# Optimization experiments

Measured on AMD Instinct MI355X. Metric: run time of the kernel, lower is better.

The kernel has to match this reference:

```python
import jax, jax.numpy as jnp
import numpy as np

MID = 256

def setup_inputs() -> dict:
    key = jax.random.key(0)
    ks = jax.random.split(key, 6)
    s = 1.0 / np.sqrt(MID)
    u = lambda k, shape: jax.random.uniform(k, shape, jnp.float32, -s, s)
    return {
        "W_ih": u(ks[0], (4 * MID, 2)),
        "W_hh": u(ks[1], (4 * MID, MID)),
        "b_ih": u(ks[2], (4 * MID,)),
        "b_hh": u(ks[3], (4 * MID,)),
        "W_out": u(ks[4], (1, MID)),
        "b_out": u(ks[5], (1,)),
        "sequence_dim": 48,
        "sequence_num": 512,
    }

def reference(W_ih, W_hh, b_ih, b_hh, W_out, b_out, sequence_dim, sequence_num):
    # obs is 2-D -> torch nn.LSTM treats it as UNBATCHED: (L=sequence_num, H_in=2),
    # hidden state (mid,) per layer, carried across outer iterations.
    N = sequence_num
    mid = W_hh.shape[1]
    b = b_ih + b_hh  # fuse the two LSTM biases

    def lstm(hc, obs):
        # obs: (N, 2) time-major unbatched sequence
        def step(carry, x):
            h, c = carry
            g = W_ih @ x + W_hh @ h + b          # (4*mid,)
            i, f, gg, o = jnp.split(g, 4)         # torch gate order i,f,g,o
            c = jax.nn.sigmoid(f) * c + jax.nn.sigmoid(i) * jnp.tanh(gg)
            h = jax.nn.sigmoid(o) * jnp.tanh(c)
            return (h, c), h
        hc, hs = jax.lax.scan(step, hc, obs)
        return hc, hs                              # hs: (N, mid)

    def outer(carry, k):
        hc, samp, prob = carry
        obs = jnp.concatenate([samp, prob], axis=1)  # (N, 2)
        hc, hs = lstm(hc, obs)
        p = jax.nn.sigmoid(hs @ W_out.T + b_out)     # (N, 1)
        smp = jax.random.bernoulli(k, p).astype(p.dtype)
        lp = smp * jnp.log(p) + (1.0 - smp) * jnp.log1p(-p)        # Bernoulli log_prob
        ent = -(p * jnp.log(p) + (1.0 - p) * jnp.log1p(-p))        # Bernoulli entropy
        return (hc, smp, p), (smp[:, 0], lp[:, 0], ent[:, 0])

    key = jax.random.key(42)
    keys = jax.random.split(key, sequence_dim - 1)
    h0 = (jnp.zeros((mid,), W_hh.dtype), jnp.zeros((mid,), W_hh.dtype))
    z = jnp.zeros((N, 1), W_hh.dtype)
    _, (ss, lps, ents) = jax.lax.scan(outer, (h0, z, z), keys)

    samples = jnp.concatenate([jnp.zeros((1, N), ss.dtype), ss], axis=0)  # (T, N)
    samples = samples.T.astype(jnp.int32)                                  # (N, T)
    logprobs = lps.sum(0)
    logprobs = logprobs - logprobs.mean()
    entropies = ents.mean(0)
    return samples, logprobs, entropies
```

## Files before the change

### kernel.cpp

```cpp
#include <hip/hip_runtime.h>
#include <stdint.h>


#define MID      256
#define NOUT     48
#define NSEQ     512
#define NOUTER   47
#define NSTEP    (NOUTER * NSEQ)
#define NBLK     16
#define MAGIC_V  0x1234ABCDu
#define LOG2E    1.4426950408889634f

__device__ __forceinline__ uint32_t rotl32(uint32_t x, int d) {
  return (x << d) | (x >> (32 - d));
}

__device__ __forceinline__ void threefry2x32(uint32_t k0, uint32_t k1,
                                             uint32_t x0, uint32_t x1,
                                             uint32_t& o0, uint32_t& o1) {
  uint32_t ks2 = k0 ^ k1 ^ 0x1BD11BDAu;
  uint32_t v0 = x0 + k0, v1 = x1 + k1;
#define TF_R(r) { v0 += v1; v1 = rotl32(v1, r); v1 ^= v0; }
  TF_R(13) TF_R(15) TF_R(26) TF_R(6)
  v0 += k1;  v1 += ks2 + 1u;
  TF_R(17) TF_R(29) TF_R(16) TF_R(24)
  v0 += ks2; v1 += k0 + 2u;
  TF_R(13) TF_R(15) TF_R(26) TF_R(6)
  v0 += k0;  v1 += k1 + 3u;
  TF_R(17) TF_R(29) TF_R(16) TF_R(24)
  v0 += k1;  v1 += ks2 + 4u;
  TF_R(13) TF_R(15) TF_R(26) TF_R(6)
  v0 += ks2; v1 += k0 + 5u;
#undef TF_R
  o0 = v0; o1 = v1;
}

__device__ __forceinline__ float sigf(float x) { return 1.0f / (1.0f + expf(-x)); }

__device__ __forceinline__ uint64_t packht(float h, uint32_t tag) {
  return ((uint64_t)tag << 32) | (uint64_t)__float_as_uint(h);
}

__global__ __launch_bounds__(256, 1)
void arlstm_kernel(const float* __restrict__ W_ih, const float* __restrict__ W_hh,
                   const float* __restrict__ b_ih, const float* __restrict__ b_hh,
                   const float* __restrict__ W_out, const float* __restrict__ b_out,
                   float* __restrict__ out, uint64_t* __restrict__ ws) {
  uint64_t* h_hist = ws;
  float*    obsbuf = (float*)(ws + 512 * 256);
  uint32_t* p_prog = (uint32_t*)(obsbuf + 2 * 512 * 2);
  uint32_t* magic  = p_prog + 16;

  const int tid = threadIdx.x;
  const int blk = blockIdx.x;

  __shared__ __align__(16) float hstage[256];
  __shared__ float plds[4][64];
  __shared__ float obs_lds[2];
  __shared__ float lp_acc[512];
  __shared__ float ent_acc[512];
  __shared__ float red[256];

  if (blk == NBLK) {
    __hip_atomic_store(&h_hist[tid], 0ull, __ATOMIC_RELAXED, __HIP_MEMORY_SCOPE_AGENT);
    if (tid < 16)
      __hip_atomic_store(&p_prog[tid], 0u, __ATOMIC_RELAXED, __HIP_MEMORY_SCOPE_AGENT);
    out[(tid)       * NOUT] = 0.0f;
    out[(tid + 256) * NOUT] = 0.0f;
    lp_acc[tid] = 0.0f;  lp_acc[tid + 256] = 0.0f;
    ent_acc[tid] = 0.0f; ent_acc[tid + 256] = 0.0f;
    __threadfence();
    __syncthreads();
    if (tid == 0)
      __hip_atomic_store(magic, MAGIC_V, __ATOMIC_RELEASE, __HIP_MEMORY_SCOPE_AGENT);

    const int w    = tid >> 6;
    const int lane = tid & 63;
    const float wo0 = W_out[lane * 4 + 0], wo1 = W_out[lane * 4 + 1];
    const float wo2 = W_out[lane * 4 + 2], wo3 = W_out[lane * 4 + 3];
    const float bo = b_out[0];

    for (int s = w + 1; s <= NSTEP; s += 4) {
      const int k = (s - 1) >> 9;
      const int t = (s - 1) & 511;
      uint64_t* src = h_hist + (uint64_t)(s & 511) * 256 + lane * 4;
      uint64_t v0, v1, v2, v3;
      for (;;) {
        v0 = __hip_atomic_load(src + 0, __ATOMIC_RELAXED, __HIP_MEMORY_SCOPE_AGENT);
        v1 = __hip_atomic_load(src + 1, __ATOMIC_RELAXED, __HIP_MEMORY_SCOPE_AGENT);
        v2 = __hip_atomic_load(src + 2, __ATOMIC_RELAXED, __HIP_MEMORY_SCOPE_AGENT);
        v3 = __hip_atomic_load(src + 3, __ATOMIC_RELAXED, __HIP_MEMORY_SCOPE_AGENT);
        int ok = ((uint32_t)(v0 >> 32) == (uint32_t)s) &
                 ((uint32_t)(v1 >> 32) == (uint32_t)s) &
                 ((uint32_t)(v2 >> 32) == (uint32_t)s) &
                 ((uint32_t)(v3 >> 32) == (uint32_t)s);
        if (__all(ok)) break;
      }
      float zp = fmaf(__uint_as_float((uint32_t)v0), wo0,
                 fmaf(__uint_as_float((uint32_t)v1), wo1,
                 fmaf(__uint_as_float((uint32_t)v2), wo2,
                      __uint_as_float((uint32_t)v3) * wo3)));
      zp += __shfl_xor(zp, 1);
      zp += __shfl_xor(zp, 2);
      zp += __shfl_xor(zp, 4);
      zp += __shfl_xor(zp, 8);
      zp += __shfl_xor(zp, 16);
      zp += __shfl_xor(zp, 32);
      const float p = sigf(zp + bo);

      uint32_t ka, kb, c1, c2;
      threefry2x32(0u, 42u, 0u, (uint32_t)k, ka, kb);
      threefry2x32(ka, kb, 0u, (uint32_t)t, c1, c2);
      const uint32_t bits = c1 ^ c2;
      const float u = __uint_as_float((bits >> 9) | 0x3f800000u) - 1.0f;
      const float smp = (u < p) ? 1.0f : 0.0f;

      if (lane == 0) {
        uint32_t* ob = (uint32_t*)(obsbuf + ((k + 1) & 1) * (512 * 2) + t * 2);
        __hip_atomic_store(&ob[0], __float_as_uint(smp), __ATOMIC_RELAXED, __HIP_MEMORY_SCOPE_AGENT);
        __hip_atomic_store(&ob[1], __float_as_uint(p),   __ATOMIC_RELAXED, __HIP_MEMORY_SCOPE_AGENT);
        __hip_atomic_store(&p_prog[w], (uint32_t)s, __ATOMIC_RELEASE, __HIP_MEMORY_SCOPE_AGENT);
        out[t * NOUT + (k + 1)] = smp;
        const float lg = logf(p), lg1 = log1pf(-p);
        lp_acc[t]  += (smp > 0.5f) ? lg : lg1;
        ent_acc[t] -= (p * lg + (1.0f - p) * lg1);
      }
    }
    __syncthreads();
    red[tid] = lp_acc[tid] + lp_acc[tid + 256];
    __syncthreads();
    for (int off = 128; off > 0; off >>= 1) {
      if (tid < off) red[tid] += red[tid + off];
      __syncthreads();
    }
    const float mean = red[0] * (1.0f / 512.0f);
    out[24576 + tid]        = lp_acc[tid]        - mean;
    out[24576 + 256 + tid]  = lp_acc[tid + 256]  - mean;
    out[25088 + tid]        = ent_acc[tid]       * (1.0f / 47.0f);
    out[25088 + 256 + tid]  = ent_acc[tid + 256] * (1.0f / 47.0f);
  } else {
    const int part = tid >> 6;
    const int r    = tid & 63;
    const int gate = r >> 4;
    const int jloc = r & 15;
    const int row  = gate * 256 + blk * 16 + jloc;

    float wreg[64];
#pragma unroll
    for (int c = 0; c < 64; ++c)
      wreg[c] = W_hh[row * 256 + part * 64 + c];

    float bb = 0.f, wx0 = 0.f, wx1 = 0.f, mconst = 0.f, ml = 0.f, ad = 0.f;
    if (tid < 64) {
      const int g4 = tid >> 4;
      const int rr = g4 * 256 + blk * 16 + (tid & 15);
      bb  = b_ih[rr] + b_hh[rr];
      wx0 = W_ih[rr * 2 + 0];
      wx1 = W_ih[rr * 2 + 1];
      mconst = (g4 == 2) ? (-2.0f * LOG2E) : (-LOG2E);
      ml     = (g4 == 2) ? 2.0f : 1.0f;
      ad     = (g4 == 2) ? -1.0f : 0.0f;
    }

    if (tid == 0) {
      while (__hip_atomic_load(magic, __ATOMIC_ACQUIRE, __HIP_MEMORY_SCOPE_AGENT) != MAGIC_V) {}
    }
    __syncthreads();

    float c_st = 0.0f;
    const int jglob = blk * 16 + (tid & 15);

    for (int s = 1; s <= NSTEP; ++s) {
      const int k = (s - 1) >> 9;
      const int t = (s - 1) & 511;

      float samp = 0.0f, pv = 0.0f;
      if (tid == 255 && k > 0) {
        const uint32_t X = (uint32_t)((k - 1) * 512 + t + 1);
        while (__hip_atomic_load(&p_prog[t & 3], __ATOMIC_ACQUIRE, __HIP_MEMORY_SCOPE_AGENT) < X) {}
        uint32_t* ob = (uint32_t*)(obsbuf + (k & 1) * (512 * 2) + t * 2);
        samp = __uint_as_float(__hip_atomic_load(&ob[0], __ATOMIC_RELAXED, __HIP_MEMORY_SCOPE_AGENT));
        pv   = __uint_as_float(__hip_atomic_load(&ob[1], __ATOMIC_RELAXED, __HIP_MEMORY_SCOPE_AGENT));
      }

      {
        uint64_t* src = h_hist + (uint64_t)((s - 1) & 511) * 256 + tid;
        const uint32_t want = (uint32_t)(s - 1);
        uint64_t v = __hip_atomic_load(src, __ATOMIC_RELAXED, __HIP_MEMORY_SCOPE_AGENT);
        if ((uint32_t)(v >> 32) != want) {
          uint64_t a = __hip_atomic_load(src, __ATOMIC_RELAXED, __HIP_MEMORY_SCOPE_AGENT);
          uint64_t b = __hip_atomic_load(src, __ATOMIC_RELAXED, __HIP_MEMORY_SCOPE_AGENT);
          for (;;) {
            if ((uint32_t)(a >> 32) == want) { v = a; break; }
            a = __hip_atomic_load(src, __ATOMIC_RELAXED, __HIP_MEMORY_SCOPE_AGENT);
            if ((uint32_t)(b >> 32) == want) { v = b; break; }
            b = __hip_atomic_load(src, __ATOMIC_RELAXED, __HIP_MEMORY_SCOPE_AGENT);
          }
        }
        hstage[tid] = __uint_as_float((uint32_t)v);
      }
      if (tid == 255) { obs_lds[0] = samp; obs_lds[1] = pv; }
      __syncthreads();

      float a0 = 0.f, a1 = 0.f, a2 = 0.f, a3 = 0.f;
      const float4* hs4 = (const float4*)(hstage + part * 64);
#pragma unroll
      for (int i = 0; i < 16; ++i) {
        const float4 hv = hs4[i];
        a0 = fmaf(wreg[4 * i + 0], hv.x, a0);
        a1 = fmaf(wreg[4 * i + 1], hv.y, a1);
        a2 = fmaf(wreg[4 * i + 2], hv.z, a2);
        a3 = fmaf(wreg[4 * i + 3], hv.w, a3);
      }
      plds[part][r] = (a0 + a1) + (a2 + a3);
      __syncthreads();

      if (tid < 64) {
        const float sx = obs_lds[0], px = obs_lds[1];
        const float base = wx0 * sx + wx1 * px + bb;
        const float gv = ((plds[0][tid] + plds[1][tid]) +
                          (plds[2][tid] + plds[3][tid])) + base;
        const float e   = __builtin_amdgcn_exp2f(gv * mconst);
        const float y   = __builtin_amdgcn_rcpf(1.0f + e);
        const float act = __builtin_fmaf(ml, y, ad);
        const int j = tid & 15;
        const float a_f = __shfl(act, j + 16, 64);
        const float a_g = __shfl(act, j + 32, 64);
        const float a_o = __shfl(act, j + 48, 64);
        if (tid < 16) {
          const float t1 = a_f * c_st;
          const float t2 = act * a_g;
          c_st = t1 + t2;
          const float ec = __builtin_amdgcn_exp2f(c_st * (-2.0f * LOG2E));
          const float yc = __builtin_amdgcn_rcpf(1.0f + ec);
          const float th = __builtin_fmaf(2.0f, yc, -1.0f);
          const float hnew = a_o * th;
          __hip_atomic_store(&h_hist[(uint64_t)(s & 511) * 256 + jglob],
                             packht(hnew, (uint32_t)s),
                             __ATOMIC_RELAXED, __HIP_MEMORY_SCOPE_AGENT);
        }
      }
    }
  }
}

extern "C" void kernel_launch(void* const* d_in, const int* in_sizes, int n_in,
                              void* d_out, int out_size, void* d_ws, size_t ws_size,
                              hipStream_t stream) {
  const float* W_ih  = (const float*)d_in[0];
  const float* W_hh  = (const float*)d_in[1];
  const float* b_ih  = (const float*)d_in[2];
  const float* b_hh  = (const float*)d_in[3];
  const float* W_out = (const float*)d_in[4];
  const float* b_out = (const float*)d_in[5];
  float* out = (float*)d_out;
  uint64_t* ws = (uint64_t*)d_ws;

  arlstm_kernel<<<dim3(NBLK + 1), dim3(256), 0, stream>>>(
      W_ih, W_hh, b_ih, b_hh, W_out, b_out, out, ws);
}
```

Baseline: 31.76 ms.

## Spread LSTM recurrence over 64 single-wave blocks and add clock-warming spin blocks

The recurrent matvec is redistributed from 16 blocks of 256 threads to 64 blocks that each use one 64-lane wavefront for 4 hidden units. Each lane holds a quarter of a W_hh row in float4 registers and reduces across lanes with shuffles. This removes the per-step __syncthreads and the LDS partial-sum stage from the critical serial path, at the cost of 4x more blocks polling the shared h history. Separately, 96 extra blocks run busy FMA loops until the sampler signals completion, apparently to keep the GPU at a high clock state during the latency-bound recurrence. That adds power draw and depends on all blocks being co-resident.

```diff
diff --git a/kernel.cpp b/kernel.cpp
--- a/kernel.cpp
+++ b/kernel.cpp
@@ -7,9 +7,17 @@
 #define NSEQ     512
 #define NOUTER   47
 #define NSTEP    (NOUTER * NSEQ)
-#define NBLK     16
+#define NWRK     64
+#define SAMP_BLK 64
+#define NHEAT    96
 #define MAGIC_V  0x1234ABCDu
+#define DONE_V   0x0D0E0D0Eu
 #define LOG2E    1.4426950408889634f
+
+#define AL_RELAX(p)    __hip_atomic_load((p), __ATOMIC_RELAXED, __HIP_MEMORY_SCOPE_AGENT)
+#define AL_ACQ(p)      __hip_atomic_load((p), __ATOMIC_ACQUIRE, __HIP_MEMORY_SCOPE_AGENT)
+#define AS_RELAX(p, v) __hip_atomic_store((p), (v), __ATOMIC_RELAXED, __HIP_MEMORY_SCOPE_AGENT)
+#define AS_REL(p, v)   __hip_atomic_store((p), (v), __ATOMIC_RELEASE, __HIP_MEMORY_SCOPE_AGENT)
 
 __device__ __forceinline__ uint32_t rotl32(uint32_t x, int d) {
   return (x << d) | (x >> (32 - d));
@@ -50,29 +58,43 @@
   float*    obsbuf = (float*)(ws + 512 * 256);
   uint32_t* p_prog = (uint32_t*)(obsbuf + 2 * 512 * 2);
   uint32_t* magic  = p_prog + 16;
+  uint32_t* done   = p_prog + 17;
+  float*    heat   = (float*)(p_prog + 32);
 
   const int tid = threadIdx.x;
   const int blk = blockIdx.x;
 
-  __shared__ __align__(16) float hstage[256];
-  __shared__ float plds[4][64];
-  __shared__ float obs_lds[2];
+  __shared__ __align__(16) float4 hstage4[64];
   __shared__ float lp_acc[512];
   __shared__ float ent_acc[512];
   __shared__ float red[256];
 
-  if (blk == NBLK) {
-    __hip_atomic_store(&h_hist[tid], 0ull, __ATOMIC_RELAXED, __HIP_MEMORY_SCOPE_AGENT);
-    if (tid < 16)
-      __hip_atomic_store(&p_prog[tid], 0u, __ATOMIC_RELAXED, __HIP_MEMORY_SCOPE_AGENT);
+  if (blk >= NWRK + 1) {
+    float h0 = (float)tid * 1.1f + 0.1f, h1 = h0 + 0.7f, h2 = h0 + 1.3f, h3 = h0 + 2.9f;
+    const float ca = 1.0000001f, cb = 1e-7f;
+    while (AL_RELAX(done) != DONE_V) {
+#pragma unroll 64
+      for (int i = 0; i < 1024; ++i) {
+        h0 = __builtin_fmaf(h0, ca, cb);
+        h1 = __builtin_fmaf(h1, ca, cb);
+        h2 = __builtin_fmaf(h2, ca, cb);
+        h3 = __builtin_fmaf(h3, ca, cb);
+      }
+    }
+    if (tid == 0) heat[blk - NWRK - 1 + 0] = (h0 + h1) + (h2 + h3);
+    return;
+  }
+
+  if (blk == SAMP_BLK) {
+    AS_RELAX(&h_hist[tid], 0ull);
+    if (tid < 16) AS_RELAX(&p_prog[tid], 0u);
     out[(tid)       * NOUT] = 0.0f;
     out[(tid + 256) * NOUT] = 0.0f;
     lp_acc[tid] = 0.0f;  lp_acc[tid + 256] = 0.0f;
     ent_acc[tid] = 0.0f; ent_acc[tid + 256] = 0.0f;
     __threadfence();
     __syncthreads();
-    if (tid == 0)
-      __hip_atomic_store(magic, MAGIC_V, __ATOMIC_RELEASE, __HIP_MEMORY_SCOPE_AGENT);
+    if (tid == 0) AS_REL(magic, MAGIC_V);
 
     const int w    = tid >> 6;
     const int lane = tid & 63;
@@ -86,10 +108,10 @@
       uint64_t* src = h_hist + (uint64_t)(s & 511) * 256 + lane * 4;
       uint64_t v0, v1, v2, v3;
       for (;;) {
-        v0 = __hip_atomic_load(src + 0, __ATOMIC_RELAXED, __HIP_MEMORY_SCOPE_AGENT);
-        v1 = __hip_atomic_load(src + 1, __ATOMIC_RELAXED, __HIP_MEMORY_SCOPE_AGENT);
-        v2 = __hip_atomic_load(src + 2, __ATOMIC_RELAXED, __HIP_MEMORY_SCOPE_AGENT);
-        v3 = __hip_atomic_load(src + 3, __ATOMIC_RELAXED, __HIP_MEMORY_SCOPE_AGENT);
+        v0 = AL_RELAX(src + 0);
+        v1 = AL_RELAX(src + 1);
+        v2 = AL_RELAX(src + 2);
+        v3 = AL_RELAX(src + 3);
         int ok = ((uint32_t)(v0 >> 32) == (uint32_t)s) &
                  ((uint32_t)(v1 >> 32) == (uint32_t)s) &
                  ((uint32_t)(v2 >> 32) == (uint32_t)s) &
@@ -117,9 +139,9 @@
 
       if (lane == 0) {
         uint32_t* ob = (uint32_t*)(obsbuf + ((k + 1) & 1) * (512 * 2) + t * 2);
-        __hip_atomic_store(&ob[0], __float_as_uint(smp), __ATOMIC_RELAXED, __HIP_MEMORY_SCOPE_AGENT);
-        __hip_atomic_store(&ob[1], __float_as_uint(p),   __ATOMIC_RELAXED, __HIP_MEMORY_SCOPE_AGENT);
-        __hip_atomic_store(&p_prog[w], (uint32_t)s, __ATOMIC_RELEASE, __HIP_MEMORY_SCOPE_AGENT);
+        AS_RELAX(&ob[0], __float_as_uint(smp));
+        AS_RELAX(&ob[1], __float_as_uint(p));
+        AS_REL(&p_prog[w], (uint32_t)s);
         out[t * NOUT + (k + 1)] = smp;
         const float lg = logf(p), lg1 = log1pf(-p);
         lp_acc[t]  += (smp > 0.5f) ? lg : lg1;
@@ -138,108 +160,111 @@
     out[24576 + 256 + tid]  = lp_acc[tid + 256]  - mean;
     out[25088 + tid]        = ent_acc[tid]       * (1.0f / 47.0f);
     out[25088 + 256 + tid]  = ent_acc[tid + 256] * (1.0f / 47.0f);
-  } else {
-    const int part = tid >> 6;
-    const int r    = tid & 63;
-    const int gate = r >> 4;
-    const int jloc = r & 15;
-    const int row  = gate * 256 + blk * 16 + jloc;
-
-    float wreg[64];
+    __syncthreads();
+    if (tid == 0) { __threadfence(); AS_REL(done, DONE_V); }
+    return;
+  }
+
+  if (tid >= 64) return;
+  const int l  = tid;
+  const int g  = l >> 4;
+  const int jj = (l >> 2) & 3;
+  const int q  = l & 3;
+  const int u  = l >> 2;
+  const int row = g * 256 + blk * 4 + jj;
+
+  float4 wf[16];
 #pragma unroll
-    for (int c = 0; c < 64; ++c)
-      wreg[c] = W_hh[row * 256 + part * 64 + c];
-
-    float bb = 0.f, wx0 = 0.f, wx1 = 0.f, mconst = 0.f, ml = 0.f, ad = 0.f;
-    if (tid < 64) {
-      const int g4 = tid >> 4;
-      const int rr = g4 * 256 + blk * 16 + (tid & 15);
-      bb  = b_ih[rr] + b_hh[rr];
-      wx0 = W_ih[rr * 2 + 0];
-      wx1 = W_ih[rr * 2 + 1];
-      mconst = (g4 == 2) ? (-2.0f * LOG2E) : (-LOG2E);
-      ml     = (g4 == 2) ? 2.0f : 1.0f;
-      ad     = (g4 == 2) ? -1.0f : 0.0f;
-    }
-
-    if (tid == 0) {
-      while (__hip_atomic_load(magic, __ATOMIC_ACQUIRE, __HIP_MEMORY_SCOPE_AGENT) != MAGIC_V) {}
-    }
-    __syncthreads();
-
-    float c_st = 0.0f;
-    const int jglob = blk * 16 + (tid & 15);
-
-    for (int s = 1; s <= NSTEP; ++s) {
-      const int k = (s - 1) >> 9;
-      const int t = (s - 1) & 511;
-
-      float samp = 0.0f, pv = 0.0f;
-      if (tid == 255 && k > 0) {
-        const uint32_t X = (uint32_t)((k - 1) * 512 + t + 1);
-        while (__hip_atomic_load(&p_prog[t & 3], __ATOMIC_ACQUIRE, __HIP_MEMORY_SCOPE_AGENT) < X) {}
-        uint32_t* ob = (uint32_t*)(obsbuf + (k & 1) * (512 * 2) + t * 2);
-        samp = __uint_as_float(__hip_atomic_load(&ob[0], __ATOMIC_RELAXED, __HIP_MEMORY_SCOPE_AGENT));
-        pv   = __uint_as_float(__hip_atomic_load(&ob[1], __ATOMIC_RELAXED, __HIP_MEMORY_SCOPE_AGENT));
-      }
-
-      {
-        uint64_t* src = h_hist + (uint64_t)((s - 1) & 511) * 256 + tid;
-        const uint32_t want = (uint32_t)(s - 1);
-        uint64_t v = __hip_atomic_load(src, __ATOMIC_RELAXED, __HIP_MEMORY_SCOPE_AGENT);
-        if ((uint32_t)(v >> 32) != want) {
-          uint64_t a = __hip_atomic_load(src, __ATOMIC_RELAXED, __HIP_MEMORY_SCOPE_AGENT);
-          uint64_t b = __hip_atomic_load(src, __ATOMIC_RELAXED, __HIP_MEMORY_SCOPE_AGENT);
-          for (;;) {
-            if ((uint32_t)(a >> 32) == want) { v = a; break; }
-            a = __hip_atomic_load(src, __ATOMIC_RELAXED, __HIP_MEMORY_SCOPE_AGENT);
-            if ((uint32_t)(b >> 32) == want) { v = b; break; }
-            b = __hip_atomic_load(src, __ATOMIC_RELAXED, __HIP_MEMORY_SCOPE_AGENT);
-          }
+  for (int i = 0; i < 16; ++i)
+    wf[i] = ((const float4*)(W_hh + (uint64_t)row * 256 + q * 64))[i];
+
+  const float bb  = b_ih[row] + b_hh[row];
+  const float wx0 = W_ih[row * 2 + 0];
+  const float wx1 = W_ih[row * 2 + 1];
+  const float mconst = (g == 2) ? (-2.0f * LOG2E) : (-LOG2E);
+  const float ml     = (g == 2) ? 2.0f : 1.0f;
+  const float ad     = (g == 2) ? -1.0f : 0.0f;
+
+  while (AL_ACQ(magic) != MAGIC_V) {}
+
+  float c_st = 0.0f;
+  const int hidx = blk * 4 + jj;
+  const int poff = q * 64 + u * 4;
+
+  for (int s = 1; s <= NSTEP; ++s) {
+    const int k = (s - 1) >> 9;
+    const int t = (s - 1) & 511;
+
+    float sxf = 0.0f, pxf = 0.0f;
+    if (l == 63 && k > 0) {
+      const uint32_t X = (uint32_t)((k - 1) * 512 + t + 1);
+      while (AL_ACQ(&p_prog[t & 3]) < X) {}
+      uint32_t* ob = (uint32_t*)(obsbuf + (k & 1) * (512 * 2) + t * 2);
+      sxf = __uint_as_float(AL_RELAX(&ob[0]));
+      pxf = __uint_as_float(AL_RELAX(&ob[1]));
+    }
+
+    uint64_t* src = h_hist + (uint64_t)((s - 1) & 511) * 256 + poff;
+    const uint32_t want = (uint32_t)(s - 1);
+    uint64_t a0 = AL_RELAX(src + 0), a1 = AL_RELAX(src + 1);
+    uint64_t a2 = AL_RELAX(src + 2), a3 = AL_RELAX(src + 3);
+#define TAGS_OK(x0,x1,x2,x3) \
+    (((uint32_t)((x0) >> 32) == want) & ((uint32_t)((x1) >> 32) == want) & \
+     ((uint32_t)((x2) >> 32) == want) & ((uint32_t)((x3) >> 32) == want))
+    if (!__all(TAGS_OK(a0, a1, a2, a3))) {
+      uint64_t b0 = AL_RELAX(src + 0), b1 = AL_RELAX(src + 1);
+      uint64_t b2 = AL_RELAX(src + 2), b3 = AL_RELAX(src + 3);
+      for (;;) {
+        if (__all(TAGS_OK(a0, a1, a2, a3))) break;
+        a0 = AL_RELAX(src + 0); a1 = AL_RELAX(src + 1);
+        a2 = AL_RELAX(src + 2); a3 = AL_RELAX(src + 3);
+        if (__all(TAGS_OK(b0, b1, b2, b3))) {
+          a0 = b0; a1 = b1; a2 = b2; a3 = b3; break;
         }
-        hstage[tid] = __uint_as_float((uint32_t)v);
-      }
-      if (tid == 255) { obs_lds[0] = samp; obs_lds[1] = pv; }
-      __syncthreads();
-
-      float a0 = 0.f, a1 = 0.f, a2 = 0.f, a3 = 0.f;
-      const float4* hs4 = (const float4*)(hstage + part * 64);
+        b0 = AL_RELAX(src + 0); b1 = AL_RELAX(src + 1);
+        b2 = AL_RELAX(src + 2); b3 = AL_RELAX(src + 3);
+      }
+    }
+#undef TAGS_OK
+
+    hstage4[u + q * 16] = make_float4(
+        __uint_as_float((uint32_t)a0), __uint_as_float((uint32_t)a1),
+        __uint_as_float((uint32_t)a2), __uint_as_float((uint32_t)a3));
+    __asm__ volatile("s_waitcnt lgkmcnt(0)" ::: "memory");
+
+    const float4* hs = &hstage4[q * 16];
+    float p0 = 0.f, p1 = 0.f, p2 = 0.f, p3 = 0.f;
 #pragma unroll
-      for (int i = 0; i < 16; ++i) {
-        const float4 hv = hs4[i];
-        a0 = fmaf(wreg[4 * i + 0], hv.x, a0);
-        a1 = fmaf(wreg[4 * i + 1], hv.y, a1);
-        a2 = fmaf(wreg[4 * i + 2], hv.z, a2);
-        a3 = fmaf(wreg[4 * i + 3], hv.w, a3);
-      }
-      plds[part][r] = (a0 + a1) + (a2 + a3);
-      __syncthreads();
-
-      if (tid < 64) {
-        const float sx = obs_lds[0], px = obs_lds[1];
-        const float base = wx0 * sx + wx1 * px + bb;
-        const float gv = ((plds[0][tid] + plds[1][tid]) +
-                          (plds[2][tid] + plds[3][tid])) + base;
-        const float e   = __builtin_amdgcn_exp2f(gv * mconst);
-        const float y   = __builtin_amdgcn_rcpf(1.0f + e);
-        const float act = __builtin_fmaf(ml, y, ad);
-        const int j = tid & 15;
-        const float a_f = __shfl(act, j + 16, 64);
-        const float a_g = __shfl(act, j + 32, 64);
-        const float a_o = __shfl(act, j + 48, 64);
-        if (tid < 16) {
-          const float t1 = a_f * c_st;
-          const float t2 = act * a_g;
-          c_st = t1 + t2;
-          const float ec = __builtin_amdgcn_exp2f(c_st * (-2.0f * LOG2E));
-          const float yc = __builtin_amdgcn_rcpf(1.0f + ec);
-          const float th = __builtin_fmaf(2.0f, yc, -1.0f);
-          const float hnew = a_o * th;
-          __hip_atomic_store(&h_hist[(uint64_t)(s & 511) * 256 + jglob],
-                             packht(hnew, (uint32_t)s),
-                             __ATOMIC_RELAXED, __HIP_MEMORY_SCOPE_AGENT);
-        }
-      }
+    for (int i = 0; i < 16; ++i) {
+      const float4 hv = hs[i];
+      p0 = fmaf(wf[i].x, hv.x, p0);
+      p1 = fmaf(wf[i].y, hv.y, p1);
+      p2 = fmaf(wf[i].z, hv.z, p2);
+      p3 = fmaf(wf[i].w, hv.w, p3);
+    }
+    float dot = (p0 + p1) + (p2 + p3);
+    dot += __shfl_xor(dot, 1);
+    dot += __shfl_xor(dot, 2);
+
+    const float sx = __shfl(sxf, 63);
+    const float px = __shfl(pxf, 63);
+    const float gv = dot + fmaf(wx0, sx, fmaf(wx1, px, bb));
+    const float e   = __builtin_amdgcn_exp2f(gv * mconst);
+    const float y   = __builtin_amdgcn_rcpf(1.0f + e);
+    const float act = __builtin_fmaf(ml, y, ad);
+
+    const float a_f = __shfl(act, (l + 16) & 63);
+    const float a_g = __shfl(act, (l + 32) & 63);
+    const float a_o = __shfl(act, (l + 48) & 63);
+
+    if (l < 16) {
+      c_st = a_f * c_st + act * a_g;
+      const float ec = __builtin_amdgcn_exp2f(c_st * (-2.0f * LOG2E));
+      const float yc = __builtin_amdgcn_rcpf(1.0f + ec);
+      const float th = __builtin_fmaf(2.0f, yc, -1.0f);
+      const float hnew = a_o * th;
+      if (q == 0)
+        AS_RELAX(&h_hist[(uint64_t)(s & 511) * 256 + hidx], packht(hnew, (uint32_t)s));
     }
   }
 }
@@ -256,6 +281,6 @@
   float* out = (float*)d_out;
   uint64_t* ws = (uint64_t*)d_ws;
 
-  arlstm_kernel<<<dim3(NBLK + 1), dim3(256), 0, stream>>>(
+  arlstm_kernel<<<dim3(NWRK + 1 + NHEAT), dim3(256), 0, stream>>>(
       W_ih, W_hh, b_ih, b_hh, W_out, b_out, out, ws);
 }
```

After: 40.98 ms. 1.29x slower.
